# Performance work log

Measured on AMD Instinct MI355X. Metric: run time of the kernel, lower is better.

The kernel has to match this reference:

```python
import jax, jax.numpy as jnp
import numpy as np

# Hamilton product tables: out component q uses weight IDX[q,p] with sign SGN[q,p]
# applied to input component p. Components order: (r, i, j, k); weights order: (rr, ri, rj, rk).
IDX = np.array([[0, 1, 2, 3], [1, 0, 3, 2], [2, 3, 0, 1], [3, 2, 1, 0]])
SGN = np.array([[1., -1., -1., -1.], [1., 1., 1., -1.], [1., -1., 1., 1.], [1., 1., -1., 1.]], dtype=np.float32)


def _qlinear(x4, w, b):
    # x4: (B, 4, Cin4, H, W); w: (4, Cout4, Cin4); b: (4, Cout4)
    # Quaternion 1x1 conv == channel-mixing matmul with Hamilton sign structure.
    wstk = jnp.asarray(SGN)[:, :, None, None] * w[IDX]  # (4,4,Cout4,Cin4)
    out = jnp.einsum('qpoc,bpchw->bqohw', wstk, x4)
    return out + b[None, :, :, None, None]


def _qdwconv(x4, w, b):
    # x4: (B, 4, Cc, H, W); w: (4, Cc, 1, 3, 3) depthwise per-channel; b: (4, Cc)
    Cc = x4.shape[2]
    comps = [x4[:, p] for p in range(4)]  # each (B, Cc, H, W)
    outs = []
    for qc in range(4):
        acc = None
        for p in range(4):
            c = SGN[qc, p] * jax.lax.conv_general_dilated(
                comps[p], w[IDX[qc, p]], window_strides=(1, 1), padding='SAME',
                feature_group_count=Cc, dimension_numbers=('NCHW', 'OIHW', 'NCHW'))
            acc = c if acc is None else acc + c
        outs.append(acc + b[qc][None, :, None, None])
    return jnp.stack(outs, axis=1)  # (B, 4, Cc, H, W)


def setup_inputs() -> dict:
    key = jax.random.key(0)
    ks = jax.random.split(key, 4)
    B, Cc, H, W = 8, 256, 32, 32   # dim = 4*Cc = 1024
    dim = 4 * Cc
    num_heads, key_dim = 8, 128
    h = 3 * num_heads * key_dim    # 3072 total -> 768 per component
    x = jax.random.normal(ks[0], (B, Cc, 4, H, W), jnp.float32)
    w_qkv = jax.random.normal(ks[1], (4, h // 4, dim // 4), jnp.float32) * (1.0 / np.sqrt(dim))
    b_qkv = jnp.zeros((4, h // 4), jnp.float32)
    w_proj = jax.random.normal(ks[2], (4, dim // 4, dim // 4), jnp.float32) * (1.0 / np.sqrt(dim))
    b_proj = jnp.zeros((4, dim // 4), jnp.float32)
    w_pe = jax.random.normal(ks[3], (4, dim // 4, 1, 3, 3), jnp.float32) * (1.0 / 6.0)
    b_pe = jnp.zeros((4, dim // 4), jnp.float32)
    return {'x': x, 'w_qkv': w_qkv, 'b_qkv': b_qkv, 'w_proj': w_proj,
            'b_proj': b_proj, 'w_pe': w_pe, 'b_pe': b_pe}


def reference(x, w_qkv, b_qkv, w_proj, b_proj, w_pe, b_pe):
    B, Cc, Q, H, W = x.shape
    num_heads, key_dim = 8, 128
    scale = key_dim ** -0.5
    N = H * W
    xq = jnp.transpose(x, (0, 2, 1, 3, 4))            # (B, 4, Cc, H, W)
    qkv = _qlinear(xq, w_qkv, b_qkv)                  # (B, 4, 768, H, W)
    q4, k4, v4 = jnp.split(qkv, 3, axis=2)            # each (B, 4, 256, H, W)

    def to_heads(t):  # (B,4,Cc,H,W) -> (B, heads, key_dim, N)
        return t.reshape(B, 4 * Cc, N).reshape(B, num_heads, key_dim, N)

    q, k, v = to_heads(q4), to_heads(k4), to_heads(v4)
    scores = jnp.einsum('bhdn,bhdm->bhnm', q, k) * scale   # (B,H,N,N) fully materialized
    attn = jax.nn.softmax(scores, axis=-1)
    out = jnp.einsum('bhnm,bhdm->bhdn', attn, v)           # (B,H,key_dim,N)
    out4 = out.reshape(B, 4, Cc, H, W)
    out = _qlinear(out4, w_proj, b_proj) + _qdwconv(xq, w_pe, b_pe)
    return jnp.transpose(out, (0, 2, 1, 3, 4))             # (B, Cc, 4, H, W)
```

## Files before the change

### kernel.cpp

```cpp
#include <hip/hip_runtime.h>
#include <hip/hip_bf16.h>

typedef unsigned short u16;
typedef float f32x4 __attribute__((ext_vector_type(4)));
typedef __bf16 bf16x8 __attribute__((ext_vector_type(8)));
typedef unsigned short su8v __attribute__((ext_vector_type(8)));
typedef unsigned short su4v __attribute__((ext_vector_type(4)));

#define BB 8
#define NHD 8
#define DD 128
#define NN 1024
#define DIM 1024
#define H3 3072
#define MM 8192
#define PTS 72
#define QSC (0.08838834764831845f * 1.4426950408889634f)

__constant__ int   d_IDX[16] = {0,1,2,3, 1,0,3,2, 2,3,0,1, 3,2,1,0};
__constant__ float d_SGN[16] = {1.f,-1.f,-1.f,-1.f, 1.f,1.f,1.f,-1.f,
                                1.f,-1.f,1.f,1.f,  1.f,1.f,-1.f,1.f};

__device__ __forceinline__ f32x4 mfma16(su8v a, su8v b, f32x4 c) {
  return __builtin_amdgcn_mfma_f32_16x16x32_bf16(
      __builtin_bit_cast(bf16x8, a), __builtin_bit_cast(bf16x8, b), c, 0, 0, 0);
}
__device__ __forceinline__ u16 f2b(float f) {
  unsigned int u = __builtin_bit_cast(unsigned int, f);
  u += 0x7fffu + ((u >> 16) & 1u);
  return (u16)(u >> 16);
}
__device__ __forceinline__ float b2f(u16 v) {
  unsigned int u = ((unsigned int)v) << 16;
  return __builtin_bit_cast(float, u);
}
typedef const __attribute__((address_space(1))) unsigned int* gas_t;
typedef __attribute__((address_space(3))) unsigned int* las_t;
__device__ __forceinline__ void gll16(const u16* g, u16* l) {
  __builtin_amdgcn_global_load_lds((gas_t)g, (las_t)l, 16, 0, 0);
}

__global__ __launch_bounds__(256) void prep_weff(
    const float* __restrict__ wqkv, const float* __restrict__ wproj,
    u16* __restrict__ weffQ, u16* __restrict__ weffP) {
  int tid = blockIdx.x * 256 + threadIdx.x;
  int stride = gridDim.x * 256;
  for (int i = tid; i < H3 * DIM; i += stride) {
    int row = i >> 10, col = i & 1023;
    int q = row / 768, o = row - q * 768;
    int p = col >> 8, c = col & 255;
    float v = d_SGN[q * 4 + p] * wqkv[(d_IDX[q * 4 + p] * 768 + o) * 256 + c];
    if (o < 256) v *= QSC;
    weffQ[i] = f2b(v);
  }
  for (int i = tid; i < DIM * DIM; i += stride) {
    int row = i >> 10, col = i & 1023;
    int q = row >> 8, o = row & 255;
    int p = col >> 8, c = col & 255;
    weffP[i] = f2b(d_SGN[q * 4 + p] * wproj[(d_IDX[q * 4 + p] * 256 + o) * 256 + c]);
  }
}

__global__ __launch_bounds__(256) void prep_x(
    const float* __restrict__ x, u16* __restrict__ Ax) {
  int id = blockIdx.x * 256 + threadIdx.x;
  const float4* xv = (const float4*)x;
  float4 f = xv[id];
  int n4 = id & 255;
  int rem = id >> 8;
  int p = rem & 3, c = (rem >> 2) & 255, b = rem >> 10;
  int col = p * 256 + c;
  size_t rbase = (size_t)(b * 1024 + n4 * 4) * 1024 + col;
  Ax[rbase] = f2b(f.x);
  Ax[rbase + 1024] = f2b(f.y);
  Ax[rbase + 2048] = f2b(f.z);
  Ax[rbase + 3072] = f2b(f.w);
}

template <int BM, int BN>
__device__ __forceinline__ void gemm_core8(
    const u16* __restrict__ Ag, const u16* __restrict__ Bg,
    u16* As, u16* Bs, int tid, f32x4 (&acc)[4][4]) {
  constexpr int WN = BN / 64;
  constexpr int AC = BM / 64;
  constexpr int BC = BN / 64;
  constexpr int NT = 16;
  int w = tid >> 6, lane = tid & 63, l16 = lane & 15, quad = lane >> 4;
  int wm = w / WN, wn = w % WN;
  int x7 = l16 & 7;
  int srow = lane >> 3;
  int sblk = (lane & 7) ^ srow;

  auto STAGE_A = [&](int tt, int bs) {
#pragma unroll
    for (int c = 0; c < AC; ++c) {
      int r0 = c * 64 + w * 8;
      gll16(Ag + (size_t)(r0 + srow) * 1024 + tt * 64 + sblk * 8,
            As + (size_t)bs * (BM * 64) + r0 * 64);
    }
  };
  auto STAGE_B = [&](int tt, int bs) {
#pragma unroll
    for (int c = 0; c < BC; ++c) {
      int r0 = c * 64 + w * 8;
      gll16(Bg + (size_t)(r0 + srow) * 1024 + tt * 64 + sblk * 8,
            Bs + (size_t)bs * (BN * 64) + r0 * 64);
    }
  };

  STAGE_A(0, 0); STAGE_B(0, 0);
  STAGE_A(1, 1); STAGE_B(1, 1);
  asm volatile("s_waitcnt vmcnt(6)" ::: "memory");
  __builtin_amdgcn_s_barrier();

  int cur = 0, nxt = 1, stg = 2;
  for (int t = 0; t < NT; ++t) {
    const u16* At = As + (size_t)cur * (BM * 64);
    const u16* Bt = Bs + (size_t)cur * (BN * 64);
#pragma unroll
    for (int kk = 0; kk < 2; ++kk) {
      su8v af[4], bf[4];
#pragma unroll
      for (int i = 0; i < 4; ++i)
        af[i] = *(const su8v*)(At + (wm * 64 + i * 16 + l16) * 64 +
                               ((kk * 4 + quad) ^ x7) * 8);
#pragma unroll
      for (int j = 0; j < 4; ++j)
        bf[j] = *(const su8v*)(Bt + (wn * 64 + j * 16 + l16) * 64 +
                               ((kk * 4 + quad) ^ x7) * 8);
      if (t + 2 < NT) {
        if (kk == 0) STAGE_A(t + 2, stg);
        else         STAGE_B(t + 2, stg);
      }
      __builtin_amdgcn_s_setprio(1);
#pragma unroll
      for (int i = 0; i < 4; ++i)
#pragma unroll
        for (int j = 0; j < 4; ++j)
          acc[i][j] = mfma16(af[i], bf[j], acc[i][j]);
      __builtin_amdgcn_s_setprio(0);
    }
    if (t < NT - 2)       asm volatile("s_waitcnt vmcnt(6)" ::: "memory");
    else if (t == NT - 2) asm volatile("s_waitcnt vmcnt(0)" ::: "memory");
    asm volatile("" ::: "memory");
    __builtin_amdgcn_s_barrier();
    asm volatile("" ::: "memory");
    int tmp = cur; cur = nxt; nxt = stg; stg = tmp;
  }
}

__global__ __launch_bounds__(512, 2) void gemm_qkv_mfma(
    const u16* __restrict__ Ax, const u16* __restrict__ weffQ,
    const float* __restrict__ bqkv,
    u16* __restrict__ Qb, u16* __restrict__ Kb, u16* __restrict__ VbT) {
  __shared__ u16 smem[3 * 384 * 64];
  int bn0 = blockIdx.x * 256;
  int col0 = blockIdx.y * 128;
  int q = col0 / 768;
  int off = col0 - q * 768;
  int sel = off >> 8;
  int head = (q * 256 + (off & 255)) >> 7;
  int tid = threadIdx.x;
  int w = tid >> 6, lane = tid & 63, l16 = lane & 15, quad = lane >> 4;
  f32x4 acc[4][4];
#pragma unroll
  for (int i = 0; i < 4; ++i)
#pragma unroll
    for (int j = 0; j < 4; ++j) acc[i][j] = (f32x4){0.f, 0.f, 0.f, 0.f};

  if (sel == 2) {
    gemm_core8<256, 128>(Ax + (size_t)bn0 * 1024, weffQ + (size_t)col0 * 1024,
                         smem, smem + 3 * 256 * 64, tid, acc);
    int wm = w >> 1, wn = w & 1;
#pragma unroll
    for (int j = 0; j < 4; ++j) {
      int dl = wn * 64 + j * 16 + l16;
      float bias = bqkv[col0 + dl];
#pragma unroll
      for (int i = 0; i < 4; ++i) {
        int m = bn0 + wm * 64 + i * 16 + quad * 4;
        int b = m >> 10, npos = m & 1023;
        int bh = b * NHD + head;
        su4v pk;
#pragma unroll
        for (int r = 0; r < 4; ++r) pk[r] = f2b(acc[i][j][r] + bias);
        *(su4v*)(VbT + ((size_t)bh * DD + dl) * NN + npos) = pk;
      }
    }
  } else {
    gemm_core8<128, 256>(weffQ + (size_t)col0 * 1024, Ax + (size_t)bn0 * 1024,
                         smem, smem + 3 * 128 * 64, tid, acc);
    int wm = w >> 2, wn = w & 3;
    u16* dst = (sel == 0) ? Qb : Kb;
    float sc = (sel == 0) ? (float)QSC : 1.0f;
#pragma unroll
    for (int i = 0; i < 4; ++i) {
      int dbase = wm * 64 + i * 16 + quad * 4;
      float4 b4 = *(const float4*)(bqkv + col0 + dbase);
#pragma unroll
      for (int j = 0; j < 4; ++j) {
        int n = bn0 + wn * 64 + j * 16 + l16;
        int b = n >> 10, npos = n & 1023;
        int bh = b * NHD + head;
        su4v pk;
        pk[0] = f2b(acc[i][j][0] + b4.x * sc);
        pk[1] = f2b(acc[i][j][1] + b4.y * sc);
        pk[2] = f2b(acc[i][j][2] + b4.z * sc);
        pk[3] = f2b(acc[i][j][3] + b4.w * sc);
        *(su4v*)(dst + ((size_t)bh * NN + npos) * DD + dbase) = pk;
      }
    }
  }
}

__global__ __launch_bounds__(256) void attn_mfma(
    const u16* __restrict__ Qb, const u16* __restrict__ Kb,
    const u16* __restrict__ VbT, u16* __restrict__ OP,
    float* __restrict__ LS) {
  __shared__ u16 Ks[64 * 128];
  __shared__ u16 Vt[128 * 64];
  __shared__ u16 Ps[4 * 32 * PTS];
  int blk = blockIdx.x;
  int bh = blk & 63;
  int rest = blk >> 6;
  int qt = rest & 7;
  int half = rest >> 3;
  int n0 = qt * 128;
  int tid = threadIdx.x;
  int w = tid >> 6, lane = tid & 63, l16 = lane & 15, quad = lane >> 4;
  const u16* Qg = Qb + ((size_t)bh * NN + n0) * DD;
  const u16* Kg = Kb + (size_t)bh * NN * DD;
  const u16* Vg = VbT + (size_t)bh * DD * NN;
  u16* Pw = Ps + w * 32 * PTS;
  int x7 = l16 & 7;

  su8v qreg[2][4];
#pragma unroll
  for (int mi = 0; mi < 2; ++mi)
#pragma unroll
    for (int ch = 0; ch < 4; ++ch)
      qreg[mi][ch] = *(const su8v*)(Qg + (size_t)(w * 32 + mi * 16 + l16) * DD +
                                    ch * 32 + quad * 8);

  float ls[2] = {0.f, 0.f};
  f32x4 accO[2][8];
#pragma unroll
  for (int mi = 0; mi < 2; ++mi)
#pragma unroll
    for (int dt = 0; dt < 8; ++dt) accO[mi][dt] = (f32x4){0.f, 0.f, 0.f, 0.f};

  for (int kt = 0; kt < 8; ++kt) {
    int c0 = half * 512 + kt * 64;
    __syncthreads();
#pragma unroll
    for (int t = 0; t < 4; ++t) {
      int ci = w * 4 + t;
      int krow = ci * 4 + (lane >> 4);
      int kblk = (lane & 15) ^ (krow & 7);
      gll16(Kg + (size_t)(c0 + krow) * DD + kblk * 8, Ks + ci * 512);
      int dv = ci * 8 + (lane >> 3);
      int vblk = (lane & 7) ^ (dv & 7);
      gll16(Vg + (size_t)dv * NN + c0 + vblk * 8, Vt + ci * 512);
    }
    __syncthreads();

    f32x4 sacc[2][4];
#pragma unroll
    for (int mi = 0; mi < 2; ++mi)
#pragma unroll
      for (int j = 0; j < 4; ++j) sacc[mi][j] = (f32x4){0.f, 0.f, 0.f, 0.f};
#pragma unroll
    for (int j = 0; j < 4; ++j) {
#pragma unroll
      for (int ch = 0; ch < 4; ++ch) {
        su8v kf = *(const su8v*)(Ks + (j * 16 + l16) * 128 +
                                 (((ch * 4 + quad) ^ x7) * 8));
        sacc[0][j] = mfma16(kf, qreg[0][ch], sacc[0][j]);
        sacc[1][j] = mfma16(kf, qreg[1][ch], sacc[1][j]);
      }
    }

#pragma unroll
    for (int mi = 0; mi < 2; ++mi)
#pragma unroll
      for (int j = 0; j < 4; ++j) {
        su4v pk;
#pragma unroll
        for (int r = 0; r < 4; ++r) {
          float p = __builtin_exp2f(sacc[mi][j][r]);
          ls[mi] += p;
          pk[r] = (u16)(__builtin_bit_cast(unsigned int, p) >> 16);
        }
        *(su4v*)(Pw + (mi * 16 + l16) * PTS + j * 16 + quad * 4) = pk;
      }

#pragma unroll
    for (int ch = 0; ch < 2; ++ch) {
      su8v pf0 = *(const su8v*)(Pw + l16 * PTS + ch * 32 + quad * 8);
      su8v pf1 = *(const su8v*)(Pw + (16 + l16) * PTS + ch * 32 + quad * 8);
#pragma unroll
      for (int dt = 0; dt < 8; ++dt) {
        su8v vf = *(const su8v*)(Vt + (dt * 16 + l16) * 64 +
                                 (((ch * 4 + quad) ^ x7) * 8));
        accO[0][dt] = mfma16(pf0, vf, accO[0][dt]);
        accO[1][dt] = mfma16(pf1, vf, accO[1][dt]);
      }
    }
  }

#pragma unroll
  for (int mi = 0; mi < 2; ++mi) {
    float s = ls[mi];
    s += __shfl_xor(s, 16, 64);
    s += __shfl_xor(s, 32, 64);
    ls[mi] = s;
  }
  size_t hb = (size_t)(half * 64 + bh);
  if (quad == 0) {
#pragma unroll
    for (int mi = 0; mi < 2; ++mi)
      LS[hb * NN + n0 + w * 32 + mi * 16 + l16] = ls[mi];
  }
#pragma unroll
  for (int mi = 0; mi < 2; ++mi)
#pragma unroll
    for (int r = 0; r < 4; ++r) {
      int row = w * 32 + mi * 16 + quad * 4 + r;
      size_t base = (hb * NN + n0 + row) * DD;
#pragma unroll
      for (int dt = 0; dt < 8; ++dt)
        OP[base + dt * 16 + l16] = f2b(accO[mi][dt][r]);
    }
}

__global__ __launch_bounds__(256) void attn_merge(
    const u16* __restrict__ OP, const float* __restrict__ LS,
    u16* __restrict__ AO) {
  size_t idx = (size_t)blockIdx.x * 256 + threadIdx.x;
  size_t e = idx * 4;
  int d = (int)(e & 127);
  size_t bhn = e >> 7;
  su4v a = *(const su4v*)(OP + bhn * DD + d);
  su4v b = *(const su4v*)(OP + (size_t)64 * NN * DD + bhn * DD + d);
  float inv = 1.0f / (LS[bhn] + LS[bhn + 64 * NN]);
  int bh = (int)(bhn >> 10), n = (int)(bhn & 1023);
  int bb = bh >> 3, head = bh & 7;
  su4v o;
#pragma unroll
  for (int r = 0; r < 4; ++r) o[r] = f2b((b2f(a[r]) + b2f(b[r])) * inv);
  *(su4v*)(AO + ((size_t)(bb * 1024 + n) * 1024) + head * 128 + d) = o;
}

__global__ __launch_bounds__(256) void qdwconv_kernel(
    const float* __restrict__ x, const float* __restrict__ wpe,
    const float* __restrict__ bpe, float* __restrict__ pe) {
  int blk = blockIdx.x;
  int co = blk & 255;
  int b = blk >> 8;
  __shared__ float pl[4][34 * 34];
  __shared__ float wsm[4][9];
  int tid = threadIdx.x;
  for (int i = tid; i < 4 * 34 * 34; i += 256) ((float*)pl)[i] = 0.f;
  if (tid < 36) wsm[tid / 9][tid % 9] = wpe[((tid / 9) * 256 + co) * 9 + tid % 9];
  __syncthreads();
  for (int i = tid; i < 4 * 1024; i += 256) {
    int p = i >> 10, n = i & 1023;
    int h = n >> 5, ww = n & 31;
    pl[p][(h + 1) * 34 + (ww + 1)] =
        x[(((size_t)b * 256 + co) * 4 + p) * 1024 + n];
  }
  __syncthreads();
  for (int n = tid; n < 1024; n += 256) {
    int h = n >> 5, ww = n & 31;
    float in[4][9];
#pragma unroll
    for (int p = 0; p < 4; ++p)
#pragma unroll
      for (int t = 0; t < 9; ++t)
        in[p][t] = pl[p][(h + t / 3) * 34 + (ww + t % 3)];
#pragma unroll
    for (int q = 0; q < 4; ++q) {
      float acc = bpe[q * 256 + co];
#pragma unroll
      for (int p = 0; p < 4; ++p) {
        int idx = d_IDX[q * 4 + p];
        float s = d_SGN[q * 4 + p];
        float sub = 0.f;
#pragma unroll
        for (int t = 0; t < 9; ++t) sub += in[p][t] * wsm[idx][t];
        acc += s * sub;
      }
      pe[(((size_t)b * 256 + co) * 4 + q) * 1024 + n] = acc;
    }
  }
}

__global__ __launch_bounds__(512, 2) void gemm_proj_mfma(
    const u16* __restrict__ AO, const u16* __restrict__ weffP,
    const float* __restrict__ bproj, const float* __restrict__ pe,
    float* __restrict__ out) {
  __shared__ u16 smem[3 * 384 * 64];
  int n0 = blockIdx.x * 256;
  int m0 = blockIdx.y * 128;
  int tid = threadIdx.x;
  f32x4 acc[4][4];
#pragma unroll
  for (int i = 0; i < 4; ++i)
#pragma unroll
    for (int j = 0; j < 4; ++j) acc[i][j] = (f32x4){0.f, 0.f, 0.f, 0.f};
  gemm_core8<128, 256>(weffP + (size_t)m0 * 1024, AO + (size_t)n0 * 1024,
                       smem, smem + 3 * 128 * 64, tid, acc);

  int w = tid >> 6, lane = tid & 63, l16 = lane & 15, quad = lane >> 4;
  int wm = w >> 2, wn = w & 3;
#pragma unroll
  for (int i = 0; i < 4; ++i) {
#pragma unroll
    for (int r = 0; r < 4; ++r) {
      int mrow = m0 + wm * 64 + i * 16 + quad * 4 + r;
      int q = mrow >> 8, o = mrow & 255;
      float bias = bproj[mrow];
#pragma unroll
      for (int j = 0; j < 4; ++j) {
        int n = n0 + wn * 64 + j * 16 + l16;
        int b = n >> 10, npos = n & 1023;
        size_t oidx = (((size_t)b * 256 + o) * 4 + q) * 1024 + npos;
        out[oidx] = pe[oidx] + acc[i][j][r] + bias;
      }
    }
  }
}

extern "C" void kernel_launch(void* const* d_in, const int* in_sizes, int n_in,
                              void* d_out, int out_size, void* d_ws,
                              size_t ws_size, hipStream_t stream) {
  const float* x      = (const float*)d_in[0];
  const float* w_qkv  = (const float*)d_in[1];
  const float* b_qkv  = (const float*)d_in[2];
  const float* w_proj = (const float*)d_in[3];
  const float* b_proj = (const float*)d_in[4];
  const float* w_pe   = (const float*)d_in[5];
  const float* b_pe   = (const float*)d_in[6];
  float* out = (float*)d_out;

  u16* ws = (u16*)d_ws;
  u16* weffQ = ws;
  u16* weffP = weffQ + (size_t)H3 * DIM;
  u16* Ax    = weffP + (size_t)DIM * DIM;
  u16* Qb    = Ax + (size_t)MM * DIM;
  u16* Kb    = Qb + (size_t)BB * NHD * NN * DD;
  u16* VbT   = Kb + (size_t)BB * NHD * NN * DD;
  u16* AO    = VbT + (size_t)BB * NHD * DD * NN;
  float* PE  = (float*)(AO + (size_t)MM * DIM);
  u16* OP    = (u16*)(PE + (size_t)MM * DIM);
  float* LS  = (float*)(OP + (size_t)2 * 64 * NN * DD);

  hipLaunchKernelGGL(prep_weff, dim3(4096), dim3(256), 0, stream,
                     w_qkv, w_proj, weffQ, weffP);
  hipLaunchKernelGGL(prep_x, dim3(8192), dim3(256), 0, stream, x, Ax);
  hipLaunchKernelGGL(gemm_qkv_mfma, dim3(MM / 256, H3 / 128), dim3(512), 0,
                     stream, Ax, weffQ, b_qkv, Qb, Kb, VbT);
  hipLaunchKernelGGL(attn_mfma, dim3(1024), dim3(256), 0, stream,
                     Qb, Kb, VbT, OP, LS);
  hipLaunchKernelGGL(attn_merge, dim3((64 * NN * DD) / (256 * 4)), dim3(256),
                     0, stream, OP, LS, AO);
  hipLaunchKernelGGL(qdwconv_kernel, dim3(BB * 256), dim3(256), 0, stream,
                     x, w_pe, b_pe, PE);
  hipLaunchKernelGGL(gemm_proj_mfma, dim3(MM / 256, DIM / 128), dim3(512), 0,
                     stream, AO, weffP, b_proj, PE, out);
}
```

Before: 314.8 us.

## Double-buffer attention K/V tiles, swizzle P scratch, and tile-transpose x prep

The attention kernel now stages K and V tiles into two shared-memory buffers, prefetching the next tile while computing on the current one and replacing the two barriers per iteration with one. It also raises wave priority around MFMA calls and replaces the padded P scratch with an XOR-swizzled layout. prep_x becomes a shared-memory tiled transpose that writes 16-byte vectors instead of scattered 2-byte stores. The costs are double the K/V LDS footprint, which may lower occupancy, and added pipeline complexity.

```diff
diff --git a/kernel.cpp b/kernel.cpp
--- a/kernel.cpp
+++ b/kernel.cpp
@@ -14,7 +14,6 @@
 #define DIM 1024
 #define H3 3072
 #define MM 8192
-#define PTS 72
 #define QSC (0.08838834764831845f * 1.4426950408889634f)
 
 __constant__ int   d_IDX[16] = {0,1,2,3, 1,0,3,2, 2,3,0,1, 3,2,1,0};
@@ -63,18 +62,35 @@
 
 __global__ __launch_bounds__(256) void prep_x(
     const float* __restrict__ x, u16* __restrict__ Ax) {
-  int id = blockIdx.x * 256 + threadIdx.x;
-  const float4* xv = (const float4*)x;
-  float4 f = xv[id];
-  int n4 = id & 255;
-  int rem = id >> 8;
-  int p = rem & 3, c = (rem >> 2) & 255, b = rem >> 10;
-  int col = p * 256 + c;
-  size_t rbase = (size_t)(b * 1024 + n4 * 4) * 1024 + col;
-  Ax[rbase] = f2b(f.x);
-  Ax[rbase + 1024] = f2b(f.y);
-  Ax[rbase + 2048] = f2b(f.z);
-  Ax[rbase + 3072] = f2b(f.w);
+  __shared__ u16 T[64 * 264];
+  int blk = blockIdx.x;
+  int nc = blk & 15;
+  int cc = (blk >> 4) & 3;
+  int b = blk >> 6;
+  int n0 = nc * 64, c0 = cc * 64;
+  int tid = threadIdx.x;
+  int nseg = tid & 15, rq = tid >> 4;
+#pragma unroll
+  for (int pass = 0; pass < 16; ++pass) {
+    int rr = pass * 16 + rq;
+    int p = rr >> 6, c = rr & 63;
+    float4 f = *(const float4*)(x + (((size_t)(b * 256 + c0 + c)) * 4 + p) * 1024 +
+                                n0 + nseg * 4);
+    T[(nseg * 4 + 0) * 264 + rr] = f2b(f.x);
+    T[(nseg * 4 + 1) * 264 + rr] = f2b(f.y);
+    T[(nseg * 4 + 2) * 264 + rr] = f2b(f.z);
+    T[(nseg * 4 + 3) * 264 + rr] = f2b(f.w);
+  }
+  __syncthreads();
+  int nl = tid >> 5, lc = tid & 31;
+#pragma unroll
+  for (int pass = 0; pass < 8; ++pass) {
+    int n = pass * 8 + nl;
+    su8v v = *(const su8v*)(&T[n * 264 + lc * 8]);
+    int pcl = lc * 8;
+    *(su8v*)(Ax + (size_t)(b * 1024 + n0 + n) * 1024 + (pcl >> 6) * 256 + c0 +
+             (pcl & 63)) = v;
+  }
 }
 
 template <int BM, int BN>
@@ -217,9 +233,9 @@
     const u16* __restrict__ Qb, const u16* __restrict__ Kb,
     const u16* __restrict__ VbT, u16* __restrict__ OP,
     float* __restrict__ LS) {
-  __shared__ u16 Ks[64 * 128];
-  __shared__ u16 Vt[128 * 64];
-  __shared__ u16 Ps[4 * 32 * PTS];
+  __shared__ u16 Ks[2][64 * 128];
+  __shared__ u16 Vt[2][128 * 64];
+  __shared__ u16 Ps[4 * 32 * 64];
   int blk = blockIdx.x;
   int bh = blk & 63;
   int rest = blk >> 6;
@@ -231,38 +247,45 @@
   const u16* Qg = Qb + ((size_t)bh * NN + n0) * DD;
   const u16* Kg = Kb + (size_t)bh * NN * DD;
   const u16* Vg = VbT + (size_t)bh * DD * NN;
-  u16* Pw = Ps + w * 32 * PTS;
+  u16* Pw = Ps + w * 32 * 64;
   int x7 = l16 & 7;
 
-  su8v qreg[2][4];
-#pragma unroll
-  for (int mi = 0; mi < 2; ++mi)
-#pragma unroll
-    for (int ch = 0; ch < 4; ++ch)
-      qreg[mi][ch] = *(const su8v*)(Qg + (size_t)(w * 32 + mi * 16 + l16) * DD +
-                                    ch * 32 + quad * 8);
-
-  float ls[2] = {0.f, 0.f};
-  f32x4 accO[2][8];
-#pragma unroll
-  for (int mi = 0; mi < 2; ++mi)
-#pragma unroll
-    for (int dt = 0; dt < 8; ++dt) accO[mi][dt] = (f32x4){0.f, 0.f, 0.f, 0.f};
-
-  for (int kt = 0; kt < 8; ++kt) {
+  auto STAGE = [&](int kt, int s) {
     int c0 = half * 512 + kt * 64;
-    __syncthreads();
 #pragma unroll
     for (int t = 0; t < 4; ++t) {
       int ci = w * 4 + t;
       int krow = ci * 4 + (lane >> 4);
       int kblk = (lane & 15) ^ (krow & 7);
-      gll16(Kg + (size_t)(c0 + krow) * DD + kblk * 8, Ks + ci * 512);
+      gll16(Kg + (size_t)(c0 + krow) * DD + kblk * 8, &Ks[s][ci * 512]);
       int dv = ci * 8 + (lane >> 3);
       int vblk = (lane & 7) ^ (dv & 7);
-      gll16(Vg + (size_t)dv * NN + c0 + vblk * 8, Vt + ci * 512);
-    }
-    __syncthreads();
+      gll16(Vg + (size_t)dv * NN + c0 + vblk * 8, &Vt[s][ci * 512]);
+    }
+  };
+
+  su8v qreg[2][4];
+#pragma unroll
+  for (int mi = 0; mi < 2; ++mi)
+#pragma unroll
+    for (int ch = 0; ch < 4; ++ch)
+      qreg[mi][ch] = *(const su8v*)(Qg + (size_t)(w * 32 + mi * 16 + l16) * DD +
+                                    ch * 32 + quad * 8);
+
+  float ls[2] = {0.f, 0.f};
+  f32x4 accO[2][8];
+#pragma unroll
+  for (int mi = 0; mi < 2; ++mi)
+#pragma unroll
+    for (int dt = 0; dt < 8; ++dt) accO[mi][dt] = (f32x4){0.f, 0.f, 0.f, 0.f};
+
+  STAGE(0, 0);
+  asm volatile("s_waitcnt vmcnt(0)" ::: "memory");
+  __builtin_amdgcn_s_barrier();
+
+  for (int kt = 0; kt < 8; ++kt) {
+    int s = kt & 1;
+    if (kt + 1 < 8) STAGE(kt + 1, s ^ 1);
 
     f32x4 sacc[2][4];
 #pragma unroll
@@ -273,10 +296,12 @@
     for (int j = 0; j < 4; ++j) {
 #pragma unroll
       for (int ch = 0; ch < 4; ++ch) {
-        su8v kf = *(const su8v*)(Ks + (j * 16 + l16) * 128 +
-                                 (((ch * 4 + quad) ^ x7) * 8));
+        su8v kf = *(const su8v*)(&Ks[s][(j * 16 + l16) * 128 +
+                                        (((ch * 4 + quad) ^ x7) * 8)]);
+        __builtin_amdgcn_s_setprio(1);
         sacc[0][j] = mfma16(kf, qreg[0][ch], sacc[0][j]);
         sacc[1][j] = mfma16(kf, qreg[1][ch], sacc[1][j]);
+        __builtin_amdgcn_s_setprio(0);
       }
     }
 
@@ -291,20 +316,31 @@
           ls[mi] += p;
           pk[r] = (u16)(__builtin_bit_cast(unsigned int, p) >> 16);
         }
-        *(su4v*)(Pw + (mi * 16 + l16) * PTS + j * 16 + quad * 4) = pk;
+        *(su4v*)(Pw + (mi * 16 + l16) * 64 +
+                 (((j * 2 + (quad >> 1)) ^ x7) << 3) + (quad & 1) * 4) = pk;
       }
 
 #pragma unroll
     for (int ch = 0; ch < 2; ++ch) {
-      su8v pf0 = *(const su8v*)(Pw + l16 * PTS + ch * 32 + quad * 8);
-      su8v pf1 = *(const su8v*)(Pw + (16 + l16) * PTS + ch * 32 + quad * 8);
+      su8v pf0 = *(const su8v*)(Pw + l16 * 64 + (((ch * 4 + quad) ^ x7) << 3));
+      su8v pf1 = *(const su8v*)(Pw + (16 + l16) * 64 +
+                                (((ch * 4 + quad) ^ x7) << 3));
 #pragma unroll
       for (int dt = 0; dt < 8; ++dt) {
-        su8v vf = *(const su8v*)(Vt + (dt * 16 + l16) * 64 +
-                                 (((ch * 4 + quad) ^ x7) * 8));
+        su8v vf = *(const su8v*)(&Vt[s][(dt * 16 + l16) * 64 +
+                                        (((ch * 4 + quad) ^ x7) * 8)]);
+        __builtin_amdgcn_s_setprio(1);
         accO[0][dt] = mfma16(pf0, vf, accO[0][dt]);
         accO[1][dt] = mfma16(pf1, vf, accO[1][dt]);
-      }
+        __builtin_amdgcn_s_setprio(0);
+      }
+    }
+
+    if (kt + 1 < 8) {
+      asm volatile("s_waitcnt vmcnt(0)" ::: "memory");
+      asm volatile("" ::: "memory");
+      __builtin_amdgcn_s_barrier();
+      asm volatile("" ::: "memory");
     }
   }
 
@@ -457,7 +493,7 @@
 
   hipLaunchKernelGGL(prep_weff, dim3(4096), dim3(256), 0, stream,
                      w_qkv, w_proj, weffQ, weffP);
-  hipLaunchKernelGGL(prep_x, dim3(8192), dim3(256), 0, stream, x, Ax);
+  hipLaunchKernelGGL(prep_x, dim3(512), dim3(256), 0, stream, x, Ax);
   hipLaunchKernelGGL(gemm_qkv_mfma, dim3(MM / 256, H3 / 128), dim3(512), 0,
                      stream, Ax, weffQ, b_qkv, Qb, Kb, VbT);
   hipLaunchKernelGGL(attn_mfma, dim3(1024), dim3(256), 0, stream,
```

Measured after the change: 324.2 us. 1.03x slower.
